# Optimization experiments

Measured on AMD Instinct MI355X. Metric: run time of the kernel, lower is better.

The kernel has to match this reference:

```python
import jax, jax.numpy as jnp
import numpy as np

L, V, Tctx, D, H, DFF = 4, 32000, 1024, 1024, 16, 4096
HD = D // H
B, T = 2, 1024


def _ln(x, w, b):
    mu = jnp.mean(x, axis=-1, keepdims=True)
    var = jnp.var(x, axis=-1, keepdims=True)
    return (x - mu) * jax.lax.rsqrt(var + 1e-5) * w + b


def setup_inputs() -> dict:
    key = jax.random.key(0)
    ks = jax.random.split(key, 8)
    s = 0.02
    return {
        "idx": jax.random.randint(ks[0], (B, T), 0, V),
        "wte": jax.random.normal(ks[1], (V, D), jnp.float32) * s,
        "wpe": jax.random.normal(ks[2], (Tctx, D), jnp.float32) * s,
        "ln1_w": jnp.ones((L, D), jnp.float32),
        "ln1_b": jnp.zeros((L, D), jnp.float32),
        "qkv_w": jax.random.normal(ks[3], (L, 3 * D, D), jnp.float32) * s,
        "qkv_b": jnp.zeros((L, 3 * D), jnp.float32),
        "proj_w": jax.random.normal(ks[4], (L, D, D), jnp.float32) * s,
        "proj_b": jnp.zeros((L, D), jnp.float32),
        "ln2_w": jnp.ones((L, D), jnp.float32),
        "ln2_b": jnp.zeros((L, D), jnp.float32),
        "fc1_w": jax.random.normal(ks[5], (L, DFF, D), jnp.float32) * s,
        "fc1_b": jnp.zeros((L, DFF), jnp.float32),
        "fc2_w": jax.random.normal(ks[6], (L, D, DFF), jnp.float32) * s,
        "fc2_b": jnp.zeros((L, D), jnp.float32),
        "lnf_w": jnp.ones((D,), jnp.float32),
        "lnf_b": jnp.zeros((D,), jnp.float32),
    }


def reference(idx, wte, wpe, ln1_w, ln1_b, qkv_w, qkv_b, proj_w, proj_b,
              ln2_w, ln2_b, fc1_w, fc1_b, fc2_w, fc2_b, lnf_w, lnf_b):
    b, t = idx.shape
    x = wte[idx] + wpe[:t]  # (B,T,D); dropout=0 (eval)
    scale = 1.0 / jnp.sqrt(jnp.float32(HD))
    causal = jnp.tril(jnp.ones((t, t), bool))  # (T,T)

    def block(x, p):
        (l1w, l1b, qw, qb, pw, pb, l2w, l2b, f1w, f1b, f2w, f2b) = p
        h = _ln(x, l1w, l1b)
        qkv = h @ qw.T + qb  # (B,T,3D)
        q, k, v = jnp.split(qkv, 3, axis=-1)
        q = q.reshape(b, t, H, HD)
        k = k.reshape(b, t, H, HD)
        v = v.reshape(b, t, H, HD)
        att = jnp.einsum('bqhd,bkhd->bhqk', q, k) * scale
        att = jnp.where(causal, att, -jnp.inf)
        att = jax.nn.softmax(att, axis=-1)
        y = jnp.einsum('bhqk,bkhd->bqhd', att, v).reshape(b, t, D)
        x = x + y @ pw.T + pb
        h2 = _ln(x, l2w, l2b)
        h2 = jax.nn.gelu(h2 @ f1w.T + f1b, approximate=False)
        x = x + h2 @ f2w.T + f2b
        return x, None

    params = (ln1_w, ln1_b, qkv_w, qkv_b, proj_w, proj_b,
              ln2_w, ln2_b, fc1_w, fc1_b, fc2_w, fc2_b)
    x, _ = jax.lax.scan(block, x, params)
    x = _ln(x, lnf_w, lnf_b)
    logits = x @ wte.T  # weight-tied lm_head
    return logits
```

## Files before the change

kernel.cpp:

```cpp
#include <hip/hip_runtime.h>
#include <hip/hip_bf16.h>
#include <cstdint>
#include <cstddef>

using hb = __hip_bfloat16;
typedef __bf16 bf16x8 __attribute__((ext_vector_type(8)));
typedef float f32x4 __attribute__((ext_vector_type(4)));
typedef const __attribute__((address_space(1))) void* gptr_t;
typedef __attribute__((address_space(3))) void* lptr_t;

namespace {
constexpr int L_ = 4, V_ = 32000, D_ = 1024, H_ = 16, DFF_ = 4096, HD_ = 64;
constexpr int B_ = 2, T_ = 1024;
constexpr int BT = B_ * T_;
constexpr int PSTR = 56;
constexpr int MTILES = BT / 128;
}

__global__ __launch_bounds__(256) void k_cast_bf16(const float* __restrict__ in,
                                                   hb* __restrict__ out, int n4) {
  int i = blockIdx.x * 256 + threadIdx.x;
  const int stride = gridDim.x * 256;
  for (; i < n4; i += stride) {
    float4 v = reinterpret_cast<const float4*>(in)[i];
    union { hb h[4]; ushort4 u; } t;
    t.h[0] = __float2bfloat16(v.x);
    t.h[1] = __float2bfloat16(v.y);
    t.h[2] = __float2bfloat16(v.z);
    t.h[3] = __float2bfloat16(v.w);
    reinterpret_cast<ushort4*>(out)[i] = t.u;
  }
}

__global__ __launch_bounds__(256) void k_embed(const int* __restrict__ idx,
                                               const float* __restrict__ wte,
                                               const float* __restrict__ wpe,
                                               float* __restrict__ x) {
  const int i = blockIdx.x * 256 + threadIdx.x;
  const int row = i >> 10;
  const int d = i & 1023;
  const int t = row & (T_ - 1);
  const int tok = idx[row];
  x[i] = wte[(size_t)tok * D_ + d] + wpe[(size_t)t * D_ + d];
}

__global__ __launch_bounds__(256) void k_ln(const float* __restrict__ x,
                                            const float* __restrict__ w,
                                            const float* __restrict__ b,
                                            hb* __restrict__ out) {
  const int row = blockIdx.x;
  const int tid = threadIdx.x;
  const float4 v = reinterpret_cast<const float4*>(x + (size_t)row * D_)[tid];
  float s = v.x + v.y + v.z + v.w;
  float ss = v.x * v.x + v.y * v.y + v.z * v.z + v.w * v.w;
#pragma unroll
  for (int o = 32; o; o >>= 1) { s += __shfl_xor(s, o); ss += __shfl_xor(ss, o); }
  __shared__ float rs[4], rss[4];
  const int wid = tid >> 6;
  if ((tid & 63) == 0) { rs[wid] = s; rss[wid] = ss; }
  __syncthreads();
  s = rs[0] + rs[1] + rs[2] + rs[3];
  ss = rss[0] + rss[1] + rss[2] + rss[3];
  const float mu = s * (1.f / D_);
  const float var = ss * (1.f / D_) - mu * mu;
  const float rstd = rsqrtf(var + 1e-5f);
  const float4 wv = reinterpret_cast<const float4*>(w)[tid];
  const float4 bv = reinterpret_cast<const float4*>(b)[tid];
  union { hb h[4]; ushort4 u; } t;
  t.h[0] = __float2bfloat16((v.x - mu) * rstd * wv.x + bv.x);
  t.h[1] = __float2bfloat16((v.y - mu) * rstd * wv.y + bv.y);
  t.h[2] = __float2bfloat16((v.z - mu) * rstd * wv.z + bv.z);
  t.h[3] = __float2bfloat16((v.w - mu) * rstd * wv.w + bv.w);
  reinterpret_cast<ushort4*>(out + (size_t)row * D_)[tid] = t.u;
}

__global__ __launch_bounds__(256) void k_vtrans(const hb* __restrict__ qkv,
                                                hb* __restrict__ vt) {
  __shared__ __align__(16) hb tile[64][66];
  const int bh = blockIdx.x;
  const int b = bh >> 4, h = bh & (H_ - 1);
  const int t0 = blockIdx.y * 64;
  const int tid = threadIdx.x;
  const int tl = tid >> 2, dc = (tid & 3) * 16;
  const hb* src = qkv + ((size_t)(b * T_ + t0 + tl) * 3 * D_) + 2 * D_ + h * HD_ + dc;
  *reinterpret_cast<bf16x8*>(&tile[tl][dc]) = *reinterpret_cast<const bf16x8*>(src);
  *reinterpret_cast<bf16x8*>(&tile[tl][dc + 8]) = *reinterpret_cast<const bf16x8*>(src + 8);
  __syncthreads();
  const int d = tid & 63, tj = tid >> 6;
  hb o[16];
#pragma unroll
  for (int j = 0; j < 16; ++j) o[j] = tile[tj * 16 + j][d];
  bf16x8* dst = reinterpret_cast<bf16x8*>(vt + ((size_t)bh * HD_ + d) * T_ + t0 + tj * 16);
  dst[0] = *reinterpret_cast<bf16x8*>(&o[0]);
  dst[1] = *reinterpret_cast<bf16x8*>(&o[8]);
}

__global__ __launch_bounds__(256) void k_attn(const hb* __restrict__ qkv,
                                              const hb* __restrict__ vt,
                                              hb* __restrict__ y) {
  const int lane = threadIdx.x & 63;
  const int wid = threadIdx.x >> 6;
  const int gw = blockIdx.x * 4 + wid;
  const int qt = 63 - (gw & 63);
  const int bh = gw >> 6;
  const int h = bh & (H_ - 1), b = bh >> 4;
  const int q0 = qt * 16;
  const int lr = lane & 15, g = lane >> 4;

  __shared__ __align__(16) hb plds[4][16 * PSTR];
  hb* pw = plds[wid];

  const size_t qrow = ((size_t)(b * T_ + q0 + lr) * 3 * D_) + (size_t)h * HD_;
  const bf16x8 qa0 = *reinterpret_cast<const bf16x8*>(qkv + qrow + g * 8);
  const bf16x8 qa1 = *reinterpret_cast<const bf16x8*>(qkv + qrow + 32 + g * 8);

  const f32x4 z = {0.f, 0.f, 0.f, 0.f};
  float m[4] = {-1e30f, -1e30f, -1e30f, -1e30f};
  float lsum[4] = {0.f, 0.f, 0.f, 0.f};
  f32x4 o[4];
#pragma unroll
  for (int i = 0; i < 4; ++i) o[i] = z;

  const int nkv = (q0 + 47) >> 5;
  for (int kt = 0; kt < nkv; ++kt) {
    const int kv0 = kt * 32;
    f32x4 s[2];
#pragma unroll
    for (int nt = 0; nt < 2; ++nt) {
      const size_t krow =
          ((size_t)(b * T_ + kv0 + nt * 16 + lr) * 3 * D_) + D_ + (size_t)h * HD_;
      const bf16x8 kb0 = *reinterpret_cast<const bf16x8*>(qkv + krow + g * 8);
      const bf16x8 kb1 = *reinterpret_cast<const bf16x8*>(qkv + krow + 32 + g * 8);
      f32x4 acc = z;
      acc = __builtin_amdgcn_mfma_f32_16x16x32_bf16(qa0, kb0, acc, 0, 0, 0);
      acc = __builtin_amdgcn_mfma_f32_16x16x32_bf16(qa1, kb1, acc, 0, 0, 0);
      s[nt] = acc;
    }
#pragma unroll
    for (int r = 0; r < 4; ++r) {
      const int qg = q0 + g * 4 + r;
      const float s0 = (kv0 + lr <= qg) ? s[0][r] * 0.125f : -1e30f;
      const float s1 = (kv0 + 16 + lr <= qg) ? s[1][r] * 0.125f : -1e30f;
      float rmax = fmaxf(s0, s1);
#pragma unroll
      for (int off = 1; off < 16; off <<= 1) rmax = fmaxf(rmax, __shfl_xor(rmax, off));
      const float mn = fmaxf(m[r], rmax);
      const float c = __expf(m[r] - mn);
      m[r] = mn;
      const float p0 = __expf(s0 - mn);
      const float p1 = __expf(s1 - mn);
      float ps = p0 + p1;
#pragma unroll
      for (int off = 1; off < 16; off <<= 1) ps += __shfl_xor(ps, off);
      lsum[r] = lsum[r] * c + ps;
#pragma unroll
      for (int dt = 0; dt < 4; ++dt) o[dt][r] *= c;
      pw[(g * 4 + r) * PSTR + lr] = __float2bfloat16(p0);
      pw[(g * 4 + r) * PSTR + 16 + lr] = __float2bfloat16(p1);
    }
    const bf16x8 pa = *reinterpret_cast<const bf16x8*>(&pw[lr * PSTR + g * 8]);
#pragma unroll
    for (int dt = 0; dt < 4; ++dt) {
      const bf16x8 vb = *reinterpret_cast<const bf16x8*>(
          vt + ((size_t)bh * HD_ + dt * 16 + lr) * T_ + kv0 + g * 8);
      o[dt] = __builtin_amdgcn_mfma_f32_16x16x32_bf16(pa, vb, o[dt], 0, 0, 0);
    }
  }
#pragma unroll
  for (int dt = 0; dt < 4; ++dt) {
#pragma unroll
    for (int r = 0; r < 4; ++r) {
      const size_t oo =
          ((size_t)(b * T_ + q0 + g * 4 + r) * D_) + h * HD_ + dt * 16 + lr;
      y[oo] = __float2bfloat16(o[dt][r] / lsum[r]);
    }
  }
}

template <int EPI, bool OBF, int BN>
__global__ __launch_bounds__(256) void gemm_bt(const hb* __restrict__ A,
                                               const hb* __restrict__ Bw,
                                               const float* __restrict__ bias,
                                               const float* resid,
                                               void* outv, int M, int N, int K) {
  constexpr int WMR = (BN == 128) ? 4 : 2;
  __shared__ __align__(16) hb As[2][128 * 32];
  __shared__ __align__(16) hb Bs[2][BN * 32];
  const int tid = threadIdx.x, lane = tid & 63, wid = tid >> 6;

  const int nwg = gridDim.x;
  const int d = blockIdx.x;
  const int wg = (d & 7) * (nwg >> 3) + (d >> 3);
  const int m0 = (wg & (MTILES - 1)) * 128;
  const int n0 = (wg / MTILES) * BN;

  const int wr = (BN == 128) ? (wid >> 1) : wid;
  const int wc = (BN == 128) ? (wid & 1) : 0;

  f32x4 acc[WMR][4];
  const f32x4 z = {0.f, 0.f, 0.f, 0.f};
#pragma unroll
  for (int i = 0; i < WMR; ++i)
#pragma unroll
    for (int j = 0; j < 4; ++j) acc[i][j] = z;

  const int e0 = tid * 8;
  auto stage = [&](int buf, int k0) {
#pragma unroll
    for (int r = 0; r < 2; ++r) {
      const int e = e0 + r * 2048;
      const int row = e >> 5, col = e & 31;
      __builtin_amdgcn_global_load_lds(
          (gptr_t)(A + (size_t)(m0 + row) * K + k0 + col), (lptr_t)(&As[buf][e]), 16, 0, 0);
    }
#pragma unroll
    for (int r = 0; r < BN / 64; ++r) {
      const int e = e0 + r * 2048;
      const int row = e >> 5, col = e & 31;
      __builtin_amdgcn_global_load_lds(
          (gptr_t)(Bw + (size_t)(n0 + row) * K + k0 + col), (lptr_t)(&Bs[buf][e]), 16, 0, 0);
    }
  };

  stage(0, 0);
  stage(1, 32);

  const int nt = K >> 5;
  const int lr = lane & 15, lk = (lane >> 4) * 8;
  for (int t = 0; t < nt; ++t) {
    const int cur = t & 1;
    if (t + 1 < nt) {
      if constexpr (BN == 128)
        asm volatile("s_waitcnt vmcnt(4)" ::: "memory");
      else
        asm volatile("s_waitcnt vmcnt(3)" ::: "memory");
    } else {
      asm volatile("s_waitcnt vmcnt(0)" ::: "memory");
    }
    asm volatile("s_barrier" ::: "memory");

    bf16x8 af[WMR], bfr[4];
#pragma unroll
    for (int i = 0; i < WMR; ++i)
      af[i] = *reinterpret_cast<const bf16x8*>(
          &As[cur][(wr * (WMR * 16) + i * 16 + lr) * 32 + lk]);
#pragma unroll
    for (int j = 0; j < 4; ++j)
      bfr[j] = *reinterpret_cast<const bf16x8*>(
          &Bs[cur][(wc * 64 + j * 16 + lr) * 32 + lk]);
#pragma unroll
    for (int i = 0; i < WMR; ++i)
#pragma unroll
      for (int j = 0; j < 4; ++j)
        acc[i][j] = __builtin_amdgcn_mfma_f32_16x16x32_bf16(af[i], bfr[j], acc[i][j], 0, 0, 0);

    asm volatile("s_waitcnt lgkmcnt(0)" ::: "memory");
    asm volatile("s_barrier" ::: "memory");
    if (t + 2 < nt) stage(cur, (t + 2) * 32);
  }

  const int lc = lane & 15, lr4 = (lane >> 4) * 4;
#pragma unroll
  for (int i = 0; i < WMR; ++i) {
    const int grow0 = m0 + wr * (WMR * 16) + i * 16 + lr4;
#pragma unroll
    for (int j = 0; j < 4; ++j) {
      const int gcol = n0 + wc * 64 + j * 16 + lc;
      const float bv = bias ? bias[gcol] : 0.f;
#pragma unroll
      for (int r = 0; r < 4; ++r) {
        const size_t oo = (size_t)(grow0 + r) * N + gcol;
        float val = acc[i][j][r] + bv;
        if constexpr (EPI == 1) val += resid[oo];
        if constexpr (EPI == 2) val = 0.5f * val * (1.f + erff(val * 0.70710678118f));
        if constexpr (OBF)
          reinterpret_cast<hb*>(outv)[oo] = __float2bfloat16(val);
        else
          reinterpret_cast<float*>(outv)[oo] = val;
      }
    }
  }
}

#define MM16(ABASE, AF, BF)                                                     \
  _Pragma("unroll") for (int i_ = 0; i_ < 4; ++i_)                              \
      _Pragma("unroll") for (int j_ = 0; j_ < 4; ++j_)                          \
          acc[(ABASE) + i_][j_] = __builtin_amdgcn_mfma_f32_16x16x32_bf16(      \
              (AF)[i_], (BF)[j_], acc[(ABASE) + i_][j_], 0, 0, 0);

__global__ __launch_bounds__(512, 2) void gemm_lmhead(const hb* __restrict__ A,
                                                      const hb* __restrict__ Bw,
                                                      float* __restrict__ out) {
  constexpr int K = 1024, N = 32000, NTK = K / 64;
  __shared__ __align__(16) hb As[2][2][256][32];
  __shared__ __align__(16) hb Bs[2][2][256][32];
  const int tid = threadIdx.x, lane = tid & 63, wid = tid >> 6;
  const int nwg = gridDim.x;
  const int dd = blockIdx.x;
  const int wg = (dd & 7) * (nwg >> 3) + (dd >> 3);
  const int m0 = (wg & 7) * 256;
  const int n0 = (wg >> 3) * 256;
  const int wr = wid >> 2, wc = wid & 3;
  const int lr = lane & 15;
  const int rc8 = (((lane >> 4) ^ ((lr >> 1) & 3)) & 3) * 8;

  f32x4 acc[8][4];
  const f32x4 z = {0.f, 0.f, 0.f, 0.f};
#pragma unroll
  for (int i = 0; i < 8; ++i)
#pragma unroll
    for (int j = 0; j < 4; ++j) acc[i][j] = z;

  const int rr = tid >> 2;
  const int cs = tid & 3;
  const int cc = cs ^ ((tid >> 3) & 3);

  auto stageA = [&](int b, int kk, int kt) {
#pragma unroll
    for (int q = 0; q < 2; ++q) {
      const int row = q * 128 + rr;
      __builtin_amdgcn_global_load_lds(
          (gptr_t)(A + (size_t)(m0 + row) * K + kt * 64 + kk * 32 + cc * 8),
          (lptr_t)(&As[b][kk][row][cs * 8]), 16, 0, 0);
    }
  };
  auto stageB = [&](int b, int kk, int kt) {
#pragma unroll
    for (int q = 0; q < 2; ++q) {
      const int row = q * 128 + rr;
      __builtin_amdgcn_global_load_lds(
          (gptr_t)(Bw + (size_t)(n0 + row) * K + kt * 64 + kk * 32 + cc * 8),
          (lptr_t)(&Bs[b][kk][row][cs * 8]), 16, 0, 0);
    }
  };
  auto dsA = [&](int b, int kk, int mh, bf16x8* af) {
#pragma unroll
    for (int i = 0; i < 4; ++i)
      af[i] = *reinterpret_cast<const bf16x8*>(
          &As[b][kk][wr * 128 + mh * 64 + i * 16 + lr][rc8]);
  };
  auto dsB = [&](int b, int kk, bf16x8* bf) {
#pragma unroll
    for (int j = 0; j < 4; ++j)
      bf[j] = *reinterpret_cast<const bf16x8*>(&Bs[b][kk][wc * 64 + j * 16 + lr][rc8]);
  };

  auto ktile = [&](int c, int kt, bool st, bool last) {
    bf16x8 af[4], bf[4];
    asm volatile("s_waitcnt vmcnt(4)" ::: "memory");
    __builtin_amdgcn_s_barrier();
    dsA(c, 0, 0, af);
    dsB(c, 0, bf);
    if (st) { stageA(c ^ 1, 0, kt + 1); stageB(c ^ 1, 0, kt + 1); }
    __builtin_amdgcn_s_setprio(1);
    MM16(0, af, bf)
    __builtin_amdgcn_s_setprio(0);
    __builtin_amdgcn_s_barrier();
    dsA(c, 0, 1, af);
    if (st) { stageA(c ^ 1, 1, kt + 1); stageB(c ^ 1, 1, kt + 1); }
    __builtin_amdgcn_s_setprio(1);
    MM16(4, af, bf)
    __builtin_amdgcn_s_setprio(0);
    __builtin_amdgcn_s_barrier();
    if (last)
      asm volatile("s_waitcnt vmcnt(0)" ::: "memory");
    else
      asm volatile("s_waitcnt vmcnt(8)" ::: "memory");
    __builtin_amdgcn_s_barrier();
    dsA(c, 1, 0, af);
    dsB(c, 1, bf);
    __builtin_amdgcn_s_setprio(1);
    MM16(0, af, bf)
    __builtin_amdgcn_s_setprio(0);
    __builtin_amdgcn_s_barrier();
    dsA(c, 1, 1, af);
    __builtin_amdgcn_s_setprio(1);
    MM16(4, af, bf)
    __builtin_amdgcn_s_setprio(0);
    __builtin_amdgcn_s_barrier();
  };

  stageA(0, 0, 0);
  stageB(0, 0, 0);
  stageA(0, 1, 0);
  stageB(0, 1, 0);

  for (int t = 0; t < NTK - 2; t += 2) {
    ktile(0, t, true, false);
    ktile(1, t + 1, true, false);
  }
  ktile(0, NTK - 2, true, false);
  ktile(1, NTK - 1, false, true);

  const int lc = lane & 15, lr4 = (lane >> 4) * 4;
#pragma unroll
  for (int i2 = 0; i2 < 8; ++i2) {
    const int grow0 = m0 + wr * 128 + i2 * 16 + lr4;
#pragma unroll
    for (int j = 0; j < 4; ++j) {
      const int gcol = n0 + wc * 64 + j * 16 + lc;
#pragma unroll
      for (int r = 0; r < 4; ++r)
        out[(size_t)(grow0 + r) * N + gcol] = acc[i2][j][r];
    }
  }
}

extern "C" void kernel_launch(void* const* d_in, const int* in_sizes, int n_in,
                              void* d_out, int out_size, void* d_ws, size_t ws_size,
                              hipStream_t stream) {
  const int* idx = (const int*)d_in[0];
  const float* wte = (const float*)d_in[1];
  const float* wpe = (const float*)d_in[2];
  const float* ln1_w = (const float*)d_in[3];
  const float* ln1_b = (const float*)d_in[4];
  const float* qkv_w = (const float*)d_in[5];
  const float* qkv_b = (const float*)d_in[6];
  const float* proj_w = (const float*)d_in[7];
  const float* proj_b = (const float*)d_in[8];
  const float* ln2_w = (const float*)d_in[9];
  const float* ln2_b = (const float*)d_in[10];
  const float* fc1_w = (const float*)d_in[11];
  const float* fc1_b = (const float*)d_in[12];
  const float* fc2_w = (const float*)d_in[13];
  const float* fc2_b = (const float*)d_in[14];
  const float* lnf_w = (const float*)d_in[15];
  const float* lnf_b = (const float*)d_in[16];

  char* ws = (char*)d_ws;
  size_t off = 0;
  auto alloc = [&](size_t bytes) -> void* {
    void* p = ws + off;
    off += (bytes + 255) & ~(size_t)255;
    return p;
  };
  hb* wte_bf = (hb*)alloc((size_t)V_ * D_ * 2);
  hb* qkvw_bf = (hb*)alloc((size_t)L_ * 3 * D_ * D_ * 2);
  hb* projw_bf = (hb*)alloc((size_t)L_ * D_ * D_ * 2);
  hb* fc1w_bf = (hb*)alloc((size_t)L_ * DFF_ * D_ * 2);
  hb* fc2w_bf = (hb*)alloc((size_t)L_ * D_ * DFF_ * 2);
  float* x = (float*)alloc((size_t)BT * D_ * 4);
  hb* hbuf = (hb*)alloc((size_t)BT * D_ * 2);
  hb* qkvbuf = (hb*)alloc((size_t)BT * 3 * D_ * 2);
  hb* ybuf = (hb*)alloc((size_t)BT * D_ * 2);
  hb* gbuf = (hb*)alloc((size_t)BT * DFF_ * 2);
  hb* vtbuf = (hb*)alloc((size_t)B_ * H_ * HD_ * T_ * 2);

  auto cast = [&](const float* src, hb* dst, size_t n) {
    int n4 = (int)(n / 4);
    int blocks = (n4 + 255) / 256;
    if (blocks > 4096) blocks = 4096;
    k_cast_bf16<<<blocks, 256, 0, stream>>>(src, dst, n4);
  };
  cast(wte, wte_bf, (size_t)V_ * D_);
  cast(qkv_w, qkvw_bf, (size_t)L_ * 3 * D_ * D_);
  cast(proj_w, projw_bf, (size_t)L_ * D_ * D_);
  cast(fc1_w, fc1w_bf, (size_t)L_ * DFF_ * D_);
  cast(fc2_w, fc2w_bf, (size_t)L_ * D_ * DFF_);

  k_embed<<<BT * D_ / 256, 256, 0, stream>>>(idx, wte, wpe, x);

  for (int l = 0; l < L_; ++l) {
    k_ln<<<BT, 256, 0, stream>>>(x, ln1_w + l * D_, ln1_b + l * D_, hbuf);
    gemm_bt<0, true, 128><<<MTILES * (3 * D_ / 128), 256, 0, stream>>>(
        hbuf, qkvw_bf + (size_t)l * 3 * D_ * D_, qkv_b + (size_t)l * 3 * D_, nullptr,
        qkvbuf, BT, 3 * D_, D_);
    k_vtrans<<<dim3(B_ * H_, T_ / 64), 256, 0, stream>>>(qkvbuf, vtbuf);
    k_attn<<<(B_ * H_ * (T_ / 16)) / 4, 256, 0, stream>>>(qkvbuf, vtbuf, ybuf);
    gemm_bt<1, false, 64><<<MTILES * (D_ / 64), 256, 0, stream>>>(
        ybuf, projw_bf + (size_t)l * D_ * D_, proj_b + (size_t)l * D_, x, x, BT, D_, D_);
    k_ln<<<BT, 256, 0, stream>>>(x, ln2_w + l * D_, ln2_b + l * D_, hbuf);
    gemm_bt<2, true, 128><<<MTILES * (DFF_ / 128), 256, 0, stream>>>(
        hbuf, fc1w_bf + (size_t)l * DFF_ * D_, fc1_b + (size_t)l * DFF_, nullptr,
        gbuf, BT, DFF_, D_);
    gemm_bt<1, false, 64><<<MTILES * (D_ / 64), 256, 0, stream>>>(
        gbuf, fc2w_bf + (size_t)l * D_ * DFF_, fc2_b + (size_t)l * D_, x, x, BT, D_, DFF_);
  }

  k_ln<<<BT, 256, 0, stream>>>(x, lnf_w, lnf_b, hbuf);
  gemm_lmhead<<<8 * (V_ / 256), 512, 0, stream>>>(hbuf, wte_bf, (float*)d_out);
}
```

Before: 1.228 ms.

## Restructure LM-head GEMM into a 4-stage K=32 LDS pipeline

Replaces the double-buffered 64-wide K tiles with a four-slot ring of 32-wide K slices in the LM-head GEMM, prefetching three slices ahead. Each slice is loaded three iterations before use and the vmcnt waits are tuned to that depth, so global loads get more lead time. LDS use stays the same. The cost is more barriers per unit of K and more complex waitcnt bookkeeping, which could serialize more.

```diff
diff --git a/kernel.cpp b/kernel.cpp
--- a/kernel.cpp
+++ b/kernel.cpp
@@ -291,9 +291,9 @@
 __global__ __launch_bounds__(512, 2) void gemm_lmhead(const hb* __restrict__ A,
                                                       const hb* __restrict__ Bw,
                                                       float* __restrict__ out) {
-  constexpr int K = 1024, N = 32000, NTK = K / 64;
-  __shared__ __align__(16) hb As[2][2][256][32];
-  __shared__ __align__(16) hb Bs[2][2][256][32];
+  constexpr int K = 1024, N = 32000, NT = K / 32;
+  __shared__ __align__(16) hb As[4][256][32];
+  __shared__ __align__(16) hb Bs[4][256][32];
   const int tid = threadIdx.x, lane = tid & 63, wid = tid >> 6;
   const int nwg = gridDim.x;
   const int dd = blockIdx.x;
@@ -315,82 +315,75 @@
   const int cs = tid & 3;
   const int cc = cs ^ ((tid >> 3) & 3);
 
-  auto stageA = [&](int b, int kk, int kt) {
+  auto stageA = [&](int b, int t) {
 #pragma unroll
     for (int q = 0; q < 2; ++q) {
       const int row = q * 128 + rr;
       __builtin_amdgcn_global_load_lds(
-          (gptr_t)(A + (size_t)(m0 + row) * K + kt * 64 + kk * 32 + cc * 8),
-          (lptr_t)(&As[b][kk][row][cs * 8]), 16, 0, 0);
-    }
-  };
-  auto stageB = [&](int b, int kk, int kt) {
+          (gptr_t)(A + (size_t)(m0 + row) * K + t * 32 + cc * 8),
+          (lptr_t)(&As[b][row][cs * 8]), 16, 0, 0);
+    }
+  };
+  auto stageB = [&](int b, int t) {
 #pragma unroll
     for (int q = 0; q < 2; ++q) {
       const int row = q * 128 + rr;
       __builtin_amdgcn_global_load_lds(
-          (gptr_t)(Bw + (size_t)(n0 + row) * K + kt * 64 + kk * 32 + cc * 8),
-          (lptr_t)(&Bs[b][kk][row][cs * 8]), 16, 0, 0);
-    }
-  };
-  auto dsA = [&](int b, int kk, int mh, bf16x8* af) {
+          (gptr_t)(Bw + (size_t)(n0 + row) * K + t * 32 + cc * 8),
+          (lptr_t)(&Bs[b][row][cs * 8]), 16, 0, 0);
+    }
+  };
+  auto dsA = [&](int b, int mh, bf16x8* af) {
 #pragma unroll
     for (int i = 0; i < 4; ++i)
       af[i] = *reinterpret_cast<const bf16x8*>(
-          &As[b][kk][wr * 128 + mh * 64 + i * 16 + lr][rc8]);
-  };
-  auto dsB = [&](int b, int kk, bf16x8* bf) {
+          &As[b][wr * 128 + mh * 64 + i * 16 + lr][rc8]);
+  };
+  auto dsB = [&](int b, bf16x8* bf) {
 #pragma unroll
     for (int j = 0; j < 4; ++j)
-      bf[j] = *reinterpret_cast<const bf16x8*>(&Bs[b][kk][wc * 64 + j * 16 + lr][rc8]);
-  };
-
-  auto ktile = [&](int c, int kt, bool st, bool last) {
+      bf[j] = *reinterpret_cast<const bf16x8*>(&Bs[b][wc * 64 + j * 16 + lr][rc8]);
+  };
+
+  auto tile = [&](int t, bool stg, int vm) {
+    const int c = t & 3;
+    const int b3 = (t + 3) & 3;
     bf16x8 af[4], bf[4];
-    asm volatile("s_waitcnt vmcnt(4)" ::: "memory");
+    dsA(c, 0, af);
+    dsB(c, bf);
+    if (stg) stageA(b3, t + 3);
     __builtin_amdgcn_s_barrier();
-    dsA(c, 0, 0, af);
-    dsB(c, 0, bf);
-    if (st) { stageA(c ^ 1, 0, kt + 1); stageB(c ^ 1, 0, kt + 1); }
+    asm volatile("s_waitcnt lgkmcnt(0)" ::: "memory");
     __builtin_amdgcn_s_setprio(1);
     MM16(0, af, bf)
     __builtin_amdgcn_s_setprio(0);
     __builtin_amdgcn_s_barrier();
-    dsA(c, 0, 1, af);
-    if (st) { stageA(c ^ 1, 1, kt + 1); stageB(c ^ 1, 1, kt + 1); }
+    dsA(c, 1, af);
+    if (stg) stageB(b3, t + 3);
+    if (vm == 8)
+      asm volatile("s_waitcnt vmcnt(8)" ::: "memory");
+    else if (vm == 4)
+      asm volatile("s_waitcnt vmcnt(4)" ::: "memory");
+    else if (vm == 0)
+      asm volatile("s_waitcnt vmcnt(0)" ::: "memory");
+    __builtin_amdgcn_s_barrier();
+    asm volatile("s_waitcnt lgkmcnt(0)" ::: "memory");
     __builtin_amdgcn_s_setprio(1);
     MM16(4, af, bf)
     __builtin_amdgcn_s_setprio(0);
     __builtin_amdgcn_s_barrier();
-    if (last)
-      asm volatile("s_waitcnt vmcnt(0)" ::: "memory");
-    else
-      asm volatile("s_waitcnt vmcnt(8)" ::: "memory");
-    __builtin_amdgcn_s_barrier();
-    dsA(c, 1, 0, af);
-    dsB(c, 1, bf);
-    __builtin_amdgcn_s_setprio(1);
-    MM16(0, af, bf)
-    __builtin_amdgcn_s_setprio(0);
-    __builtin_amdgcn_s_barrier();
-    dsA(c, 1, 1, af);
-    __builtin_amdgcn_s_setprio(1);
-    MM16(4, af, bf)
-    __builtin_amdgcn_s_setprio(0);
-    __builtin_amdgcn_s_barrier();
-  };
-
-  stageA(0, 0, 0);
-  stageB(0, 0, 0);
-  stageA(0, 1, 0);
-  stageB(0, 1, 0);
-
-  for (int t = 0; t < NTK - 2; t += 2) {
-    ktile(0, t, true, false);
-    ktile(1, t + 1, true, false);
-  }
-  ktile(0, NTK - 2, true, false);
-  ktile(1, NTK - 1, false, true);
+  };
+
+  stageA(0, 0); stageB(0, 0);
+  stageA(1, 1); stageB(1, 1);
+  stageA(2, 2); stageB(2, 2);
+  asm volatile("s_waitcnt vmcnt(8)" ::: "memory");
+  __builtin_amdgcn_s_barrier();
+
+  for (int t = 0; t < NT - 3; ++t) tile(t, true, 8);
+  tile(NT - 3, false, 4);
+  tile(NT - 2, false, 0);
+  tile(NT - 1, false, -1);
 
   const int lc = lane & 15, lr4 = (lane >> 4) * 4;
 #pragma unroll
```

Measured after the change: 1.214 ms. No clear change (-1.2%).
